# Performance work log

Hardware: AMD Instinct MI355X
Metric: run time of the kernel (lower is better)

The kernel has to match this reference:

```python
import jax, jax.numpy as jnp
import numpy as np

B, K, D, H = 16, 256, 256, 128

def setup_inputs() -> dict:
    key = jax.random.key(0)
    k1, k2, k3 = jax.random.split(key, 3)
    x = jax.random.normal(k1, (B, K, D), dtype=jnp.float32)
    # Linear(2D, H): weight stored as (2D, H) for x @ W convention
    W1 = jax.random.normal(k2, (2 * D, H), dtype=jnp.float32) * (1.0 / np.sqrt(2 * D))
    b1 = jnp.zeros((H,), dtype=jnp.float32)
    W2 = jax.random.normal(k3, (H, D), dtype=jnp.float32) * (1.0 / np.sqrt(H))
    b2 = jnp.zeros((D,), dtype=jnp.float32)
    return {"x": x, "W1": W1, "b1": b1, "W2": W2, "b2": b2}

def reference(x, W1, b1, W2, b2):
    # Original: for each i, concat([x_i broadcast, x_j]) -> Linear -> ReLU -> Linear -> mean_j, + residual.
    # Split the first Linear over the concat: W1 = [W1a; W1b], so
    # pre-act(i,j) = x_i @ W1a + x_j @ W1b + b1  (avoids materializing the concat).
    D_ = x.shape[-1]
    W1a, W1b = W1[:D_], W1[D_:]
    a = jnp.einsum('bkd,dh->bkh', x, W1a)            # B x K x H (query side)
    b = jnp.einsum('bkd,dh->bkh', x, W1b)            # B x K x H (key side)
    h = jax.nn.relu(a[:, :, None, :] + b[:, None, :, :] + b1)  # B x K x K x H
    mh = h.mean(axis=2)                               # mean over j; Linear commutes with mean
    out = jnp.einsum('bkh,hd->bkd', mh, W2) + b2      # B x K x D
    return out + x
```

## Files before the change

kernel.cpp:

```cpp
#include <hip/hip_runtime.h>

#define NM 4096
#define NH 128
#define ND 256
#define STR 260

typedef __attribute__((ext_vector_type(8))) short bf16x8;
typedef __attribute__((ext_vector_type(4))) float f32x4;

__device__ __forceinline__ unsigned short f2bf(float f) {
  unsigned u = __float_as_uint(f);
  u += 0x7FFFu + ((u >> 16) & 1u);
  return (unsigned short)(u >> 16);
}

__global__ __launch_bounds__(512) void kA(
    const float* __restrict__ x, const float* __restrict__ W1,
    const float* __restrict__ b1, unsigned short* __restrict__ mhb)
{
  __shared__ __align__(16) unsigned char smem[131072 + 2 * 8320];
  unsigned short* xs = (unsigned short*)smem;
  float* As = (float*)(smem + 131072);
  float* Cs = (float*)(smem + 131072 + 8320);

  const int tid = threadIdx.x, lane = tid & 63, wu = tid >> 6;
  const int b = blockIdx.x, hc = blockIdx.y;
  const int h0 = hc * 8;
  const int fr = lane & 15, fq = lane >> 4;

  const float* __restrict__ wp =
      W1 + (size_t)((fr >= 8) ? 256 : 0) * NH + h0 + (fr & 7);
  bf16x8 afr[8];
#pragma unroll
  for (int c = 0; c < 8; ++c) {
    union { bf16x8 v; unsigned short s[8]; } t;
#pragma unroll
    for (int j = 0; j < 8; ++j)
      t.s[j] = f2bf(wp[(size_t)(c * 32 + fq * 8 + j) * NH]);
    afr[c] = t.v;
  }

#pragma unroll 8
  for (int i = 0; i < 32; ++i) {
    const int idx = i * 512 + tid;
    const int row = idx >> 6, u = idx & 63;
    float4 v = *(const float4*)&x[(size_t)(b * 256 + row) * 256 + u * 4];
    ushort4 hv = make_ushort4(f2bf(v.x), f2bf(v.y), f2bf(v.z), f2bf(v.w));
    *(ushort4*)&xs[row * 256 + (u ^ ((row & 7) << 1)) * 4] = hv;
  }
  __syncthreads();

  float b1v[4] = {0.f, 0.f, 0.f, 0.f};
  if (fq >= 2) {
#pragma unroll
    for (int g = 0; g < 4; ++g) b1v[g] = b1[h0 + (fq - 2) * 4 + g];
  }

#pragma unroll
  for (int ts = 0; ts < 2; ++ts) {
    const int mrow = (wu * 2 + ts) * 16 + fr;
    const int swz = (mrow & 7) << 1;
    f32x4 acc = {0.f, 0.f, 0.f, 0.f};
#pragma unroll
    for (int c = 0; c < 8; ++c) {
      const int pu = (c * 8 + fq * 2) ^ swz;
      bf16x8 bfr = *(const bf16x8*)&xs[mrow * 256 + pu * 4];
      acc = __builtin_amdgcn_mfma_f32_16x16x32_bf16(afr[c], bfr, acc, 0, 0, 0);
    }
    if (fq < 2) {
#pragma unroll
      for (int g = 0; g < 4; ++g) As[(fq * 4 + g) * STR + mrow] = acc[g];
    } else {
#pragma unroll
      for (int g = 0; g < 4; ++g)
        Cs[((fq - 2) * 4 + g) * STR + mrow] = acc[g] + b1v[g];
    }
  }
  __syncthreads();

  const float* __restrict__ Arow = As + wu * STR;
  const float* __restrict__ Crow = Cs + wu * STR;
  const float a0 = Arow[lane];
  const float a1 = Arow[64 + lane];
  const float a2 = Arow[128 + lane];
  const float a3 = Arow[192 + lane];

  float4 s4 = *(const float4*)&Crow[lane * 4];
  float sumC = (s4.x + s4.y) + (s4.z + s4.w);
#pragma unroll
  for (int off = 32; off >= 1; off >>= 1) sumC += __shfl_xor(sumC, off, 64);

  float ab0a = 0.f, ab0b = 0.f, ab1a = 0.f, ab1b = 0.f;
  float ab2a = 0.f, ab2b = 0.f, ab3a = 0.f, ab3b = 0.f;
#pragma unroll 8
  for (int u = 0; u < 64; ++u) {
    float4 c = *(const float4*)&Crow[u * 4];
    ab0a += fabsf(a0 + c.x); ab0b += fabsf(a0 + c.y);
    ab0a += fabsf(a0 + c.z); ab0b += fabsf(a0 + c.w);
    ab1a += fabsf(a1 + c.x); ab1b += fabsf(a1 + c.y);
    ab1a += fabsf(a1 + c.z); ab1b += fabsf(a1 + c.w);
    ab2a += fabsf(a2 + c.x); ab2b += fabsf(a2 + c.y);
    ab2a += fabsf(a2 + c.z); ab2b += fabsf(a2 + c.w);
    ab3a += fabsf(a3 + c.x); ab3b += fabsf(a3 + c.y);
    ab3a += fabsf(a3 + c.z); ab3b += fabsf(a3 + c.w);
  }

  const float mh0 = (256.f * a0 + sumC + (ab0a + ab0b)) * (1.f / 512.f);
  const float mh1 = (256.f * a1 + sumC + (ab1a + ab1b)) * (1.f / 512.f);
  const float mh2 = (256.f * a2 + sumC + (ab2a + ab2b)) * (1.f / 512.f);
  const float mh3 = (256.f * a3 + sumC + (ab3a + ab3b)) * (1.f / 512.f);
  __syncthreads();

  As[wu * STR + lane]       = mh0;
  As[wu * STR + 64 + lane]  = mh1;
  As[wu * STR + 128 + lane] = mh2;
  As[wu * STR + 192 + lane] = mh3;
  __syncthreads();

  if (tid < 256) {
    union { uint4 v; unsigned short s[8]; } o;
#pragma unroll
    for (int j = 0; j < 8; ++j) o.s[j] = f2bf(As[j * STR + tid]);
    *(uint4*)&mhb[(size_t)(b * 256 + tid) * NH + h0] = o.v;
  }
}

__global__ __launch_bounds__(256) void kB_mfma(
    const unsigned short* __restrict__ mhb, const float* __restrict__ W2,
    const float* __restrict__ b2, const float* __restrict__ x,
    float* __restrict__ out)
{
  const int tid = threadIdx.x, lane = tid & 63, wu = tid >> 6;
  const int m0 = blockIdx.x * 32;
  const int d0 = (blockIdx.y * 4 + wu) * 16;
  const int fr = lane & 15, fq = lane >> 4;

  const float* __restrict__ w2p = W2 + d0 + fr;
  bf16x8 bfr[4];
#pragma unroll
  for (int c = 0; c < 4; ++c) {
    union { bf16x8 v; unsigned short s[8]; } t;
#pragma unroll
    for (int j = 0; j < 8; ++j)
      t.s[j] = f2bf(w2p[(size_t)(c * 32 + fq * 8 + j) * ND]);
    bfr[c] = t.v;
  }

  const float bv = b2[d0 + fr];
#pragma unroll
  for (int ms = 0; ms < 2; ++ms) {
    const unsigned short* apm = mhb + (size_t)(m0 + ms * 16 + fr) * NH + fq * 8;
    f32x4 acc = {0.f, 0.f, 0.f, 0.f};
#pragma unroll
    for (int c = 0; c < 4; ++c) {
      bf16x8 a = *(const bf16x8*)(apm + c * 32);
      acc = __builtin_amdgcn_mfma_f32_16x16x32_bf16(a, bfr[c], acc, 0, 0, 0);
    }
#pragma unroll
    for (int g = 0; g < 4; ++g) {
      const int m = m0 + ms * 16 + fq * 4 + g;
      const size_t o = (size_t)m * ND + d0 + fr;
      out[o] = acc[g] + bv + x[o];
    }
  }
}

extern "C" void kernel_launch(void* const* d_in, const int* in_sizes, int n_in,
                              void* d_out, int out_size, void* d_ws, size_t ws_size,
                              hipStream_t stream) {
  const float* x  = (const float*)d_in[0];
  const float* W1 = (const float*)d_in[1];
  const float* b1 = (const float*)d_in[2];
  const float* W2 = (const float*)d_in[3];
  const float* b2 = (const float*)d_in[4];
  float* out = (float*)d_out;

  unsigned short* mhb = (unsigned short*)d_ws;

  kA<<<dim3(16, 16), 512, 0, stream>>>(x, W1, b1, mhb);
  kB_mfma<<<dim3(128, 4), 256, 0, stream>>>(mhb, W2, b2, x, out);
}
```

Measured before the change: 25.25 us.

## Pre-pack x and weights into bf16 MFMA fragment layout in a separate kernel

Adds a pre-pass kernel that converts x, W1 and W2 to bf16 and stores them in the exact per-lane MFMA fragment order. kA then loads the fragments directly from global memory instead of staging x through a large swizzled shared-memory tile, uses 1024 threads, and splits the |a+c| reduction across two wave halves. kB also reads pre-packed fragments and its output tile per block shrinks. The aim is to cut repeated fp32-to-bf16 conversion (x was converted 16 times per batch), strided weight gathers and shared-memory pressure. The cost is an extra kernel launch plus a round trip of the packed data through global memory.

```diff
diff --git a/kernel.cpp b/kernel.cpp
--- a/kernel.cpp
+++ b/kernel.cpp
@@ -1,167 +1,176 @@
 #include <hip/hip_runtime.h>
-
-#define NM 4096
-#define NH 128
-#define ND 256
-#define STR 260
 
 typedef __attribute__((ext_vector_type(8))) short bf16x8;
 typedef __attribute__((ext_vector_type(4))) float f32x4;
+
+union FragU { uint4 q; bf16x8 h; };
 
 __device__ __forceinline__ unsigned short f2bf(float f) {
   unsigned u = __float_as_uint(f);
   u += 0x7FFFu + ((u >> 16) & 1u);
   return (unsigned short)(u >> 16);
 }
+__device__ __forceinline__ unsigned pack2(float lo, float hi) {
+  return (unsigned)f2bf(lo) | ((unsigned)f2bf(hi) << 16);
+}
 
-__global__ __launch_bounds__(512) void kA(
+__global__ __launch_bounds__(256) void kX(
     const float* __restrict__ x, const float* __restrict__ W1,
-    const float* __restrict__ b1, unsigned short* __restrict__ mhb)
+    const float* __restrict__ W2, uint4* __restrict__ xbf,
+    uint4* __restrict__ w1f, uint4* __restrict__ w2f)
 {
-  __shared__ __align__(16) unsigned char smem[131072 + 2 * 8320];
-  unsigned short* xs = (unsigned short*)smem;
-  float* As = (float*)(smem + 131072);
-  float* Cs = (float*)(smem + 131072 + 8320);
+  const int u = blockIdx.x * 256 + threadIdx.x;
+  if (u < 131072) {
+    const int l = u & 63, c = (u >> 6) & 7, t = (u >> 9) & 15, b = u >> 13;
+    const int fr = l & 15, fq = l >> 4;
+    const float* p = x + (size_t)((b * 16 + t) * 16 + fr) * 256 + c * 32 + fq * 8;
+    float4 va = *(const float4*)p;
+    float4 vb = *(const float4*)(p + 4);
+    xbf[u] = make_uint4(pack2(va.x, va.y), pack2(va.z, va.w),
+                        pack2(vb.x, vb.y), pack2(vb.z, vb.w));
+  } else if (u < 139264) {
+    const int u2 = u - 131072;
+    const int l = u2 & 63, c = (u2 >> 6) & 7, hc = u2 >> 9;
+    const int fr = l & 15, fq = l >> 4;
+    const float* p = W1 + (size_t)((fr >= 8) ? 256 : 0) * 128 +
+                     (size_t)(c * 32 + fq * 8) * 128 + hc * 8 + (fr & 7);
+    float v[8];
+#pragma unroll
+    for (int j = 0; j < 8; ++j) v[j] = p[(size_t)j * 128];
+    w1f[u2] = make_uint4(pack2(v[0], v[1]), pack2(v[2], v[3]),
+                         pack2(v[4], v[5]), pack2(v[6], v[7]));
+  } else if (u < 143360) {
+    const int u3 = u - 139264;
+    const int l = u3 & 63, c = (u3 >> 6) & 3, dg = u3 >> 8;
+    const int fr = l & 15, fq = l >> 4;
+    const float* p = W2 + (size_t)(c * 32 + fq * 8) * 256 + dg * 16 + fr;
+    float v[8];
+#pragma unroll
+    for (int j = 0; j < 8; ++j) v[j] = p[(size_t)j * 256];
+    w2f[u3] = make_uint4(pack2(v[0], v[1]), pack2(v[2], v[3]),
+                         pack2(v[4], v[5]), pack2(v[6], v[7]));
+  }
+}
 
-  const int tid = threadIdx.x, lane = tid & 63, wu = tid >> 6;
+__global__ __launch_bounds__(1024) void kA(
+    const uint4* __restrict__ xbf, const uint4* __restrict__ w1f,
+    const float* __restrict__ b1, uint4* __restrict__ mf)
+{
+  __shared__ float Cs[8][260];
+  __shared__ float As[8][260];
+  __shared__ float PB[8][260];
+
+  const int tid = threadIdx.x, lane = tid & 63, wv = tid >> 6;
   const int b = blockIdx.x, hc = blockIdx.y;
-  const int h0 = hc * 8;
   const int fr = lane & 15, fq = lane >> 4;
 
-  const float* __restrict__ wp =
-      W1 + (size_t)((fr >= 8) ? 256 : 0) * NH + h0 + (fr & 7);
-  bf16x8 afr[8];
+  FragU afr[8];
 #pragma unroll
-  for (int c = 0; c < 8; ++c) {
-    union { bf16x8 v; unsigned short s[8]; } t;
+  for (int c = 0; c < 8; ++c) afr[c].q = w1f[(hc * 8 + c) * 64 + lane];
+
+  float b1v[4];
 #pragma unroll
-    for (int j = 0; j < 8; ++j)
-      t.s[j] = f2bf(wp[(size_t)(c * 32 + fq * 8 + j) * NH]);
-    afr[c] = t.v;
-  }
+  for (int g = 0; g < 4; ++g)
+    b1v[g] = (fq >= 2) ? b1[hc * 8 + (fq - 2) * 4 + g] : 0.f;
 
-#pragma unroll 8
-  for (int i = 0; i < 32; ++i) {
-    const int idx = i * 512 + tid;
-    const int row = idx >> 6, u = idx & 63;
-    float4 v = *(const float4*)&x[(size_t)(b * 256 + row) * 256 + u * 4];
-    ushort4 hv = make_ushort4(f2bf(v.x), f2bf(v.y), f2bf(v.z), f2bf(v.w));
-    *(ushort4*)&xs[row * 256 + (u ^ ((row & 7) << 1)) * 4] = hv;
-  }
-  __syncthreads();
-
-  float b1v[4] = {0.f, 0.f, 0.f, 0.f};
-  if (fq >= 2) {
-#pragma unroll
-    for (int g = 0; g < 4; ++g) b1v[g] = b1[h0 + (fq - 2) * 4 + g];
-  }
-
-#pragma unroll
-  for (int ts = 0; ts < 2; ++ts) {
-    const int mrow = (wu * 2 + ts) * 16 + fr;
-    const int swz = (mrow & 7) << 1;
+  {
+    const int t = wv;
     f32x4 acc = {0.f, 0.f, 0.f, 0.f};
 #pragma unroll
     for (int c = 0; c < 8; ++c) {
-      const int pu = (c * 8 + fq * 2) ^ swz;
-      bf16x8 bfr = *(const bf16x8*)&xs[mrow * 256 + pu * 4];
-      acc = __builtin_amdgcn_mfma_f32_16x16x32_bf16(afr[c], bfr, acc, 0, 0, 0);
+      FragU bfr;
+      bfr.q = xbf[((size_t)(b * 16 + t) * 8 + c) * 64 + lane];
+      acc = __builtin_amdgcn_mfma_f32_16x16x32_bf16(afr[c].h, bfr.h, acc, 0, 0, 0);
     }
+    const int m = t * 16 + fr;
     if (fq < 2) {
 #pragma unroll
-      for (int g = 0; g < 4; ++g) As[(fq * 4 + g) * STR + mrow] = acc[g];
+      for (int g = 0; g < 4; ++g) As[fq * 4 + g][m] = acc[g];
     } else {
 #pragma unroll
-      for (int g = 0; g < 4; ++g)
-        Cs[((fq - 2) * 4 + g) * STR + mrow] = acc[g] + b1v[g];
+      for (int g = 0; g < 4; ++g) Cs[(fq - 2) * 4 + g][m] = acc[g] + b1v[g];
     }
   }
   __syncthreads();
 
-  const float* __restrict__ Arow = As + wu * STR;
-  const float* __restrict__ Crow = Cs + wu * STR;
-  const float a0 = Arow[lane];
-  const float a1 = Arow[64 + lane];
-  const float a2 = Arow[128 + lane];
-  const float a3 = Arow[192 + lane];
+  const int hp = wv & 7, kh = wv >> 3;
+  const float a0 = As[hp][lane],       a1 = As[hp][64 + lane];
+  const float a2 = As[hp][128 + lane], a3 = As[hp][192 + lane];
 
-  float4 s4 = *(const float4*)&Crow[lane * 4];
-  float sumC = (s4.x + s4.y) + (s4.z + s4.w);
+  float sumC = 0.f;
+  if (kh == 0) {
+    float4 s4 = *(const float4*)&Cs[hp][lane * 4];
+    sumC = (s4.x + s4.y) + (s4.z + s4.w);
 #pragma unroll
-  for (int off = 32; off >= 1; off >>= 1) sumC += __shfl_xor(sumC, off, 64);
-
-  float ab0a = 0.f, ab0b = 0.f, ab1a = 0.f, ab1b = 0.f;
-  float ab2a = 0.f, ab2b = 0.f, ab3a = 0.f, ab3b = 0.f;
-#pragma unroll 8
-  for (int u = 0; u < 64; ++u) {
-    float4 c = *(const float4*)&Crow[u * 4];
-    ab0a += fabsf(a0 + c.x); ab0b += fabsf(a0 + c.y);
-    ab0a += fabsf(a0 + c.z); ab0b += fabsf(a0 + c.w);
-    ab1a += fabsf(a1 + c.x); ab1b += fabsf(a1 + c.y);
-    ab1a += fabsf(a1 + c.z); ab1b += fabsf(a1 + c.w);
-    ab2a += fabsf(a2 + c.x); ab2b += fabsf(a2 + c.y);
-    ab2a += fabsf(a2 + c.z); ab2b += fabsf(a2 + c.w);
-    ab3a += fabsf(a3 + c.x); ab3b += fabsf(a3 + c.y);
-    ab3a += fabsf(a3 + c.z); ab3b += fabsf(a3 + c.w);
+    for (int off = 32; off >= 1; off >>= 1) sumC += __shfl_xor(sumC, off, 64);
   }
 
-  const float mh0 = (256.f * a0 + sumC + (ab0a + ab0b)) * (1.f / 512.f);
-  const float mh1 = (256.f * a1 + sumC + (ab1a + ab1b)) * (1.f / 512.f);
-  const float mh2 = (256.f * a2 + sumC + (ab2a + ab2b)) * (1.f / 512.f);
-  const float mh3 = (256.f * a3 + sumC + (ab3a + ab3b)) * (1.f / 512.f);
+  float s0a = 0.f, s0b = 0.f, s1a = 0.f, s1b = 0.f;
+  float s2a = 0.f, s2b = 0.f, s3a = 0.f, s3b = 0.f;
+  const int u0 = kh * 32;
+#pragma unroll 8
+  for (int u = 0; u < 32; ++u) {
+    float4 c = *(const float4*)&Cs[hp][(u0 + u) * 4];
+    s0a += fabsf(a0 + c.x); s0b += fabsf(a0 + c.y);
+    s0a += fabsf(a0 + c.z); s0b += fabsf(a0 + c.w);
+    s1a += fabsf(a1 + c.x); s1b += fabsf(a1 + c.y);
+    s1a += fabsf(a1 + c.z); s1b += fabsf(a1 + c.w);
+    s2a += fabsf(a2 + c.x); s2b += fabsf(a2 + c.y);
+    s2a += fabsf(a2 + c.z); s2b += fabsf(a2 + c.w);
+    s3a += fabsf(a3 + c.x); s3b += fabsf(a3 + c.y);
+    s3a += fabsf(a3 + c.z); s3b += fabsf(a3 + c.w);
+  }
+
+  if (kh == 1) {
+    PB[hp][lane]       = s0a + s0b;
+    PB[hp][64 + lane]  = s1a + s1b;
+    PB[hp][128 + lane] = s2a + s2b;
+    PB[hp][192 + lane] = s3a + s3b;
+  }
   __syncthreads();
 
-  As[wu * STR + lane]       = mh0;
-  As[wu * STR + 64 + lane]  = mh1;
-  As[wu * STR + 128 + lane] = mh2;
-  As[wu * STR + 192 + lane] = mh3;
+  if (kh == 0) {
+    As[hp][lane]       = (256.f * a0 + sumC + (s0a + s0b) + PB[hp][lane])       * (1.f / 512.f);
+    As[hp][64 + lane]  = (256.f * a1 + sumC + (s1a + s1b) + PB[hp][64 + lane])  * (1.f / 512.f);
+    As[hp][128 + lane] = (256.f * a2 + sumC + (s2a + s2b) + PB[hp][128 + lane]) * (1.f / 512.f);
+    As[hp][192 + lane] = (256.f * a3 + sumC + (s3a + s3b) + PB[hp][192 + lane]) * (1.f / 512.f);
+  }
   __syncthreads();
 
   if (tid < 256) {
-    union { uint4 v; unsigned short s[8]; } o;
-#pragma unroll
-    for (int j = 0; j < 8; ++j) o.s[j] = f2bf(As[j * STR + tid]);
-    *(uint4*)&mhb[(size_t)(b * 256 + tid) * NH + h0] = o.v;
+    const int fr2 = tid & 15, T = tid >> 4;
+    uint4 o = make_uint4(pack2(As[0][tid], As[1][tid]), pack2(As[2][tid], As[3][tid]),
+                         pack2(As[4][tid], As[5][tid]), pack2(As[6][tid], As[7][tid]));
+    mf[((size_t)(b * 16 + T) * 4 + (hc >> 2)) * 64 + (hc & 3) * 16 + fr2] = o;
   }
 }
 
-__global__ __launch_bounds__(256) void kB_mfma(
-    const unsigned short* __restrict__ mhb, const float* __restrict__ W2,
+__global__ __launch_bounds__(256) void kB(
+    const uint4* __restrict__ mf, const uint4* __restrict__ w2f,
     const float* __restrict__ b2, const float* __restrict__ x,
     float* __restrict__ out)
 {
   const int tid = threadIdx.x, lane = tid & 63, wu = tid >> 6;
-  const int m0 = blockIdx.x * 32;
-  const int d0 = (blockIdx.y * 4 + wu) * 16;
+  const int mt = blockIdx.x;
+  const int dg = blockIdx.y * 4 + wu;
   const int fr = lane & 15, fq = lane >> 4;
 
-  const float* __restrict__ w2p = W2 + d0 + fr;
-  bf16x8 bfr[4];
+  f32x4 acc = {0.f, 0.f, 0.f, 0.f};
 #pragma unroll
   for (int c = 0; c < 4; ++c) {
-    union { bf16x8 v; unsigned short s[8]; } t;
-#pragma unroll
-    for (int j = 0; j < 8; ++j)
-      t.s[j] = f2bf(w2p[(size_t)(c * 32 + fq * 8 + j) * ND]);
-    bfr[c] = t.v;
+    FragU a, bb;
+    a.q  = mf[((size_t)mt * 4 + c) * 64 + lane];
+    bb.q = w2f[((size_t)dg * 4 + c) * 64 + lane];
+    acc = __builtin_amdgcn_mfma_f32_16x16x32_bf16(a.h, bb.h, acc, 0, 0, 0);
   }
 
-  const float bv = b2[d0 + fr];
+  const int d = dg * 16 + fr;
+  const float bv = b2[d];
 #pragma unroll
-  for (int ms = 0; ms < 2; ++ms) {
-    const unsigned short* apm = mhb + (size_t)(m0 + ms * 16 + fr) * NH + fq * 8;
-    f32x4 acc = {0.f, 0.f, 0.f, 0.f};
-#pragma unroll
-    for (int c = 0; c < 4; ++c) {
-      bf16x8 a = *(const bf16x8*)(apm + c * 32);
-      acc = __builtin_amdgcn_mfma_f32_16x16x32_bf16(a, bfr[c], acc, 0, 0, 0);
-    }
-#pragma unroll
-    for (int g = 0; g < 4; ++g) {
-      const int m = m0 + ms * 16 + fq * 4 + g;
-      const size_t o = (size_t)m * ND + d0 + fr;
-      out[o] = acc[g] + bv + x[o];
-    }
+  for (int g = 0; g < 4; ++g) {
+    const int m = mt * 16 + fq * 4 + g;
+    const size_t o = (size_t)m * 256 + d;
+    out[o] = acc[g] + bv + x[o];
   }
 }
 
@@ -175,8 +184,13 @@
   const float* b2 = (const float*)d_in[4];
   float* out = (float*)d_out;
 
-  unsigned short* mhb = (unsigned short*)d_ws;
+  char* ws = (char*)d_ws;
+  uint4* xbf = (uint4*)ws;
+  uint4* w1f = (uint4*)(ws + (2u << 20));
+  uint4* w2f = (uint4*)(ws + (2u << 20) + (128u << 10));
+  uint4* mf  = (uint4*)(ws + (2u << 20) + (192u << 10));
 
-  kA<<<dim3(16, 16), 512, 0, stream>>>(x, W1, b1, mhb);
-  kB_mfma<<<dim3(128, 4), 256, 0, stream>>>(mhb, W2, b2, x, out);
+  kX<<<560, 256, 0, stream>>>(x, W1, W2, xbf, w1f, w2f);
+  kA<<<dim3(16, 16), 1024, 0, stream>>>(xbf, w1f, b1, mf);
+  kB<<<dim3(256, 4), 256, 0, stream>>>(mf, w2f, b2, x, out);
 }
```

Result: no change. 25.60 us (+1.4%).
